# Performance work log

Measured on AMD Instinct MI355X. Metric: run time of the kernel, lower is better.

## Reference

```python
import jax, jax.numpy as jnp
import numpy as np

N_SRC, N_DST, K, T = 16384, 8192, 16, 2
NODE_IN, EDGE_IN, TIME_D = 128, 64, 128
D_MODEL = NODE_IN + TIME_D + EDGE_IN  # 320
N_HEAD, D_K = 8, 64                   # d_k = d_v
HID = 128
LN_EPS = 1e-5


def setup_inputs() -> dict:
    key = jax.random.key(0)
    ks = jax.random.split(key, 10)
    std_qk = np.sqrt(2.0 / (D_MODEL + D_K)).astype(np.float32)
    return {
        "node_features": jax.random.normal(ks[0], (N_SRC, NODE_IN), jnp.float32),
        "edge_features": jax.random.normal(ks[1], (N_DST, K, T, EDGE_IN), jnp.float32),
        "delta_t": jax.random.uniform(ks[2], (N_DST, K, T), jnp.float32) * 100.0,
        "neigh_idx": jax.random.randint(ks[3], (N_DST, K), 0, N_SRC),
        "basis_freq": jnp.asarray(1.0 / 10 ** np.linspace(0, 9, TIME_D), jnp.float32),
        "phase": jnp.zeros((TIME_D,), jnp.float32),
        "w_qs": jax.random.normal(ks[4], (N_HEAD * D_K, D_MODEL), jnp.float32) * std_qk,
        "w_ks": jax.random.normal(ks[5], (N_HEAD * D_K, D_MODEL), jnp.float32) * std_qk,
        "w_vs": jax.random.normal(ks[6], (N_HEAD * D_K, D_MODEL), jnp.float32) * std_qk,
        "fc_w": jax.random.normal(ks[7], (D_MODEL, N_HEAD * D_K), jnp.float32) * 0.03,
        "fc_b": jnp.zeros((D_MODEL,), jnp.float32),
        "ln_g": jnp.ones((D_MODEL,), jnp.float32),
        "ln_b": jnp.zeros((D_MODEL,), jnp.float32),
        "node_w": jax.random.normal(ks[8], (HID, 2 * NODE_IN + TIME_D + EDGE_IN), jnp.float32) * 0.05,
        "node_b": jnp.zeros((HID,), jnp.float32),
    }


def reference(node_features, edge_features, delta_t, neigh_idx, basis_freq, phase,
              w_qs, w_ks, w_vs, fc_w, fc_b, ln_g, ln_b, node_w, node_b):
    h_dst = node_features[:N_DST]                                  # [N, NODE_IN]
    # message_func: per-edge time encoding + gather src feats + concat
    te = jnp.cos(delta_t[..., None] * basis_freq + phase)          # [N, K, T, TIME_D]
    h_nb = node_features[neigh_idx]                                # [N, K, NODE_IN] (irregular gather)
    h_nb = jnp.broadcast_to(h_nb[:, :, None, :], (N_DST, K, T, NODE_IN))
    m = jnp.concatenate([h_nb, edge_features, te], axis=-1)        # [N, K, T, D_MODEL]
    m = m.reshape(N_DST, K * T, D_MODEL)                           # mailbox kv
    # reduce_func query: [h_dst, zeros(edge_in), time_encode(0)=cos(phase)]
    t0 = jnp.broadcast_to(jnp.cos(phase), (N_DST, TIME_D))
    q = jnp.concatenate([h_dst, jnp.zeros((N_DST, EDGE_IN), h_dst.dtype), t0], axis=-1)  # [N, D_MODEL]
    # multi-head attention (len_q = 1)
    qh = (q @ w_qs.T).reshape(N_DST, N_HEAD, D_K)
    kh = (m @ w_ks.T).reshape(N_DST, K * T, N_HEAD, D_K)
    vh = (m @ w_vs.T).reshape(N_DST, K * T, N_HEAD, D_K)
    scores = jnp.einsum('nhd,nlhd->nhl', qh, kh) / np.float32(np.sqrt(D_K))
    attn = jax.nn.softmax(scores, axis=-1)
    ctx = jnp.einsum('nhl,nlhd->nhd', attn, vh).reshape(N_DST, N_HEAD * D_K)
    out = ctx @ fc_w.T + fc_b
    x = out + q                                                    # residual
    mu = x.mean(-1, keepdims=True)
    var = x.var(-1, keepdims=True)
    h_neigh = ln_g * (x - mu) * jax.lax.rsqrt(var + LN_EPS) + ln_b  # layer norm
    h = jnp.concatenate([h_dst, h_neigh], axis=-1)                 # [N, 2*NODE_IN+TIME_D+EDGE_IN]
    return jax.nn.relu(h @ node_w.T + node_b)                      # [N, HID]
```

## Files before the change

### kernel.cpp

```cpp
#include <hip/hip_runtime.h>
#include <math.h>

#define LNB      32
#define NODE_IN  128
#define EDGE_IN  64
#define TIME_D   128
#define D_MODEL  320
#define N_HEAD   8
#define D_K      64
#define NHD      512
#define HID      128
#define IN2      448
#define N_DSTN   8192

typedef __attribute__((ext_vector_type(8))) short bf16x8;
typedef __attribute__((ext_vector_type(4))) float f32x4;
#define MFMA16(a,b,c) __builtin_amdgcn_mfma_f32_16x16x32_bf16(a,b,c,0,0,0)

#define WS_WQ    0
#define WS_WKT   163840
#define WS_WV    327680
#define WS_FCW   491520
#define WS_NW    655360
#define WS_QKM   712704

__device__ __forceinline__ unsigned short f2bf(float f) {
  union { float f; unsigned i; } v; v.f = f;
  unsigned x = v.i;
  return (unsigned short)((x + 0x7fffu + ((x >> 16) & 1u)) >> 16);
}

__global__ __launch_bounds__(256)
void prep_weights(const float* __restrict__ wq, const float* __restrict__ wk,
                  const float* __restrict__ wv, const float* __restrict__ fcw,
                  const float* __restrict__ nw, unsigned short* __restrict__ ws)
{
  int i = blockIdx.x * 256 + threadIdx.x;
  ws[WS_WQ + i] = f2bf(wq[i]);
  {
    int h = i / 20480, r = i - h * 20480, d = r >> 6, dk = r & 63;
    ws[WS_WKT + i] = f2bf(wk[(size_t)(h * 64 + dk) * D_MODEL + d]);
  }
  ws[WS_WV + i] = f2bf(wv[i]);
  ws[WS_FCW + i] = f2bf(fcw[i]);
  if (i < HID * IN2) ws[WS_NW + i] = f2bf(nw[i]);
}

__global__ __launch_bounds__(256, 4)
void tgat_qk(const float* __restrict__ nf, const float* __restrict__ ph,
             const unsigned short* __restrict__ ws, unsigned short* __restrict__ qkm)
{
  __shared__ alignas(16) unsigned short sQ[16 * 328];
  __shared__ alignas(16) unsigned short sQH[16 * 520];
  __shared__ float cph[TIME_D];

  const int tid = threadIdx.x;
  const int wid = tid >> 6, lane = tid & 63, qd = lane >> 4, lm = lane & 15;
  const int n0 = blockIdx.x * 16;
  const unsigned short* wsWQ  = ws + WS_WQ;
  const unsigned short* wsWKT = ws + WS_WKT;

  if (tid < TIME_D) cph[tid] = __cosf(ph[tid]);
  __syncthreads();
  for (int k = 0; k < 20; ++k) {
    int idx = k * 256 + tid;
    int n = idx / D_MODEL, d = idx - n * D_MODEL;
    float v;
    if (d < NODE_IN)      v = nf[(size_t)(n0 + n) * NODE_IN + d];
    else if (d < 192)     v = 0.f;
    else                  v = cph[d - 192];
    sQ[n * 328 + d] = f2bf(v);
  }
  __syncthreads();

  {
    f32x4 acc[8] = {};
    for (int kt = 0; kt < 10; ++kt) {
      bf16x8 a = *(const bf16x8*)&sQ[lm * 328 + kt * 32 + qd * 8];
      #pragma unroll
      for (int u = 0; u < 8; ++u) {
        int j = (wid * 8 + u) * 16 + lm;
        bf16x8 b = *(const bf16x8*)&wsWQ[(size_t)j * D_MODEL + kt * 32 + qd * 8];
        acc[u] = MFMA16(a, b, acc[u]);
      }
    }
    #pragma unroll
    for (int u = 0; u < 8; ++u)
      #pragma unroll
      for (int r = 0; r < 4; ++r)
        sQH[(qd * 4 + r) * 520 + (wid * 8 + u) * 16 + lm] = f2bf(acc[u][r]);
  }
  __syncthreads();

  #pragma unroll
  for (int t = 0; t < 2; ++t) {
    const int h = wid + 4 * t;
    bf16x8 a0 = *(const bf16x8*)&sQH[lm * 520 + h * 64 + qd * 8];
    bf16x8 a1 = *(const bf16x8*)&sQH[lm * 520 + h * 64 + 32 + qd * 8];
    for (int dt = 0; dt < 20; ++dt) {
      int d = dt * 16 + lm;
      bf16x8 b0 = *(const bf16x8*)&wsWKT[((size_t)h * D_MODEL + d) * 64 + qd * 8];
      bf16x8 b1 = *(const bf16x8*)&wsWKT[((size_t)h * D_MODEL + d) * 64 + 32 + qd * 8];
      f32x4 acc = {};
      acc = MFMA16(a0, b0, acc);
      acc = MFMA16(a1, b1, acc);
      #pragma unroll
      for (int r = 0; r < 4; ++r)
        qkm[(size_t)(n0 + qd * 4 + r) * 2560 + h * D_MODEL + d] = f2bf(acc[r]);
    }
  }
}

__global__ __launch_bounds__(256, 3)
void tgat_attn(const float* __restrict__ nf, const float* __restrict__ ef,
               const float* __restrict__ dtp, const int* __restrict__ nidx,
               const float* __restrict__ freq, const float* __restrict__ ph,
               unsigned short* __restrict__ qkm)
{
  __shared__ alignas(16) unsigned short sM [LNB * 328];
  __shared__ alignas(16) unsigned short sMT[D_MODEL * 40];
  __shared__ alignas(16) unsigned short sATT[16 * 40];
  __shared__ float sFP[TIME_D], sPH[TIME_D], sDT[LNB];
  __shared__ int   sNI[16];

  const int tid = threadIdx.x;
  const int wid = tid >> 6, lane = tid & 63, qd = lane >> 4, lm = lane & 15;
  const int n = blockIdx.x;

  if (tid < TIME_D) { sFP[tid] = freq[tid]; sPH[tid] = ph[tid]; }
  if (tid < 16)  sNI[tid] = nidx[n * 16 + tid];
  if (tid < LNB) sDT[tid] = dtp[(size_t)n * LNB + tid];
  __syncthreads();

  #pragma unroll 1
  for (int it = 0; it < 5; ++it) {
    int g = it * 256 + tid;
    int l = g & 31, dg = g >> 5;
    int d0 = dg * 8;
    float v[8];
    if (dg < 16) {
      const float4* src = (const float4*)(nf + (size_t)sNI[l >> 1] * NODE_IN + d0);
      float4 f0 = src[0], f1 = src[1];
      v[0]=f0.x; v[1]=f0.y; v[2]=f0.z; v[3]=f0.w; v[4]=f1.x; v[5]=f1.y; v[6]=f1.z; v[7]=f1.w;
    } else if (dg < 24) {
      const float4* src = (const float4*)(ef + ((size_t)n * LNB + l) * EDGE_IN + (d0 - NODE_IN));
      float4 f0 = src[0], f1 = src[1];
      v[0]=f0.x; v[1]=f0.y; v[2]=f0.z; v[3]=f0.w; v[4]=f1.x; v[5]=f1.y; v[6]=f1.z; v[7]=f1.w;
    } else {
      int dd = d0 - 192;
      float dt = sDT[l];
      #pragma unroll
      for (int j = 0; j < 8; ++j) v[j] = __cosf(dt * sFP[dd + j] + sPH[dd + j]);
    }
    unsigned short b8[8];
    #pragma unroll
    for (int j = 0; j < 8; ++j) b8[j] = f2bf(v[j]);
    *(bf16x8*)&sM[l * 328 + d0] = *(const bf16x8*)b8;
    #pragma unroll
    for (int j = 0; j < 8; ++j) sMT[(d0 + j) * 40 + l] = b8[j];
  }
  __syncthreads();

  if (wid == 0) {
    const unsigned short* qn = qkm + (size_t)n * 2560;
    f32x4 acc0 = {}, acc1 = {};
    for (int kt = 0; kt < 10; ++kt) {
      bf16x8 b = {0,0,0,0,0,0,0,0};
      if (lm < 8) b = *(const bf16x8*)&qn[lm * D_MODEL + kt * 32 + qd * 8];
      bf16x8 a0 = *(const bf16x8*)&sM[lm * 328 + kt * 32 + qd * 8];
      bf16x8 a1 = *(const bf16x8*)&sM[(16 + lm) * 328 + kt * 32 + qd * 8];
      acc0 = MFMA16(a0, b, acc0);
      acc1 = MFMA16(a1, b, acc1);
    }
    float s[8], e[8];
    #pragma unroll
    for (int r = 0; r < 4; ++r) { s[r] = acc0[r] * 0.125f; s[4 + r] = acc1[r] * 0.125f; }
    float mx = s[0];
    #pragma unroll
    for (int i = 1; i < 8; ++i) mx = fmaxf(mx, s[i]);
    mx = fmaxf(mx, __shfl_xor(mx, 16));
    mx = fmaxf(mx, __shfl_xor(mx, 32));
    float sum = 0.f;
    #pragma unroll
    for (int i = 0; i < 8; ++i) { e[i] = __expf(s[i] - mx); sum += e[i]; }
    sum += __shfl_xor(sum, 16);
    sum += __shfl_xor(sum, 32);
    float inv = 1.f / sum;
    #pragma unroll
    for (int i = 0; i < 8; ++i) {
      int l = (i < 4) ? (qd * 4 + i) : (16 + qd * 4 + (i - 4));
      sATT[lm * 40 + l] = f2bf(e[i] * inv);
    }
  }
  __syncthreads();

  {
    bf16x8 a = *(const bf16x8*)&sATT[lm * 40 + qd * 8];
    for (int dt = wid; dt < 20; dt += 4) {
      int d = dt * 16 + lm;
      bf16x8 b = *(const bf16x8*)&sMT[d * 40 + qd * 8];
      f32x4 acc = {};
      acc = MFMA16(a, b, acc);
      if (qd < 2) {
        #pragma unroll
        for (int r = 0; r < 4; ++r)
          qkm[(size_t)n * 2560 + (qd * 4 + r) * D_MODEL + d] = f2bf(acc[r]);
      }
    }
  }
}

__global__ __launch_bounds__(256, 3)
void tgat_post(const float* __restrict__ nf, const float* __restrict__ ph,
               const float* __restrict__ fcb, const float* __restrict__ lng,
               const float* __restrict__ lnb_, const float* __restrict__ nbias,
               const unsigned short* __restrict__ ws,
               const unsigned short* __restrict__ qkm, float* __restrict__ out)
{
  __shared__ alignas(16) unsigned short sCtx[16 * 520];
  __shared__ alignas(16) float sX[16 * 321];
  __shared__ alignas(16) unsigned short sXb[16 * 328];
  __shared__ alignas(16) unsigned short sQb[16 * 136];
  __shared__ float cph[TIME_D];

  const int tid = threadIdx.x;
  const int wid = tid >> 6, lane = tid & 63, qd = lane >> 4, lm = lane & 15;
  const int n0 = blockIdx.x * 16;
  const unsigned short* wsWV  = ws + WS_WV;
  const unsigned short* wsFCW = ws + WS_FCW;
  const unsigned short* wsNW  = ws + WS_NW;

  if (tid < TIME_D) cph[tid] = __cosf(ph[tid]);
  {
    int nn = tid >> 4, k0 = (tid & 15) * 8;
    const float4* src = (const float4*)(nf + (size_t)(n0 + nn) * NODE_IN + k0);
    float4 f0 = src[0], f1 = src[1];
    unsigned short b8[8] = { f2bf(f0.x), f2bf(f0.y), f2bf(f0.z), f2bf(f0.w),
                             f2bf(f1.x), f2bf(f1.y), f2bf(f1.z), f2bf(f1.w) };
    *(bf16x8*)&sQb[nn * 136 + k0] = *(const bf16x8*)b8;
  }

  #pragma unroll
  for (int t = 0; t < 2; ++t) {
    const int h = wid + 4 * t;
    f32x4 acc[4] = {};
    for (int kt = 0; kt < 10; ++kt) {
      bf16x8 a = *(const bf16x8*)&qkm[(size_t)(n0 + lm) * 2560 + h * D_MODEL + kt * 32 + qd * 8];
      #pragma unroll
      for (int u = 0; u < 4; ++u) {
        int jv = h * 64 + u * 16 + lm;
        bf16x8 b = *(const bf16x8*)&wsWV[(size_t)jv * D_MODEL + kt * 32 + qd * 8];
        acc[u] = MFMA16(a, b, acc[u]);
      }
    }
    #pragma unroll
    for (int u = 0; u < 4; ++u)
      #pragma unroll
      for (int r = 0; r < 4; ++r)
        sCtx[(qd * 4 + r) * 520 + h * 64 + u * 16 + lm] = f2bf(acc[u][r]);
  }
  __syncthreads();

  {
    f32x4 acc[5] = {};
    for (int ks = 0; ks < 16; ++ks) {
      bf16x8 a = *(const bf16x8*)&sCtx[lm * 520 + ks * 32 + qd * 8];
      #pragma unroll
      for (int u = 0; u < 5; ++u) {
        int c = (wid + 4 * u) * 16 + lm;
        bf16x8 b = *(const bf16x8*)&wsFCW[(size_t)c * NHD + ks * 32 + qd * 8];
        acc[u] = MFMA16(a, b, acc[u]);
      }
    }
    #pragma unroll
    for (int u = 0; u < 5; ++u) {
      int c = (wid + 4 * u) * 16 + lm;
      float fb = fcb[c];
      #pragma unroll
      for (int r = 0; r < 4; ++r) {
        int nn = qd * 4 + r;
        float qv;
        if (c < NODE_IN)      qv = nf[(size_t)(n0 + nn) * NODE_IN + c];
        else if (c < 192)     qv = 0.f;
        else                  qv = cph[c - 192];
        sX[nn * 321 + c] = acc[u][r] + fb + qv;
      }
    }
  }
  __syncthreads();

  #pragma unroll
  for (int t = 0; t < 4; ++t) {
    int nn = wid * 4 + t;
    float v[5], s = 0.f, s2 = 0.f;
    #pragma unroll
    for (int i = 0; i < 5; ++i) {
      v[i] = sX[nn * 321 + lane + 64 * i];
      s += v[i]; s2 += v[i] * v[i];
    }
    #pragma unroll
    for (int off = 32; off >= 1; off >>= 1) { s += __shfl_xor(s, off); s2 += __shfl_xor(s2, off); }
    float mean = s * (1.f / D_MODEL);
    float var  = s2 * (1.f / D_MODEL) - mean * mean;
    float rstd = rsqrtf(var + 1e-5f);
    #pragma unroll
    for (int i = 0; i < 5; ++i) {
      int c = lane + 64 * i;
      sXb[nn * 328 + c] = f2bf(lng[c] * ((v[i] - mean) * rstd) + lnb_[c]);
    }
  }
  __syncthreads();

  #pragma unroll
  for (int t = 0; t < 2; ++t) {
    int o = (wid + 4 * t) * 16 + lm;
    f32x4 acc = {};
    for (int ks = 0; ks < 14; ++ks) {
      bf16x8 a;
      if (ks < 4) a = *(const bf16x8*)&sQb[lm * 136 + ks * 32 + qd * 8];
      else        a = *(const bf16x8*)&sXb[lm * 328 + (ks - 4) * 32 + qd * 8];
      bf16x8 b = *(const bf16x8*)&wsNW[(size_t)o * IN2 + ks * 32 + qd * 8];
      acc = MFMA16(a, b, acc);
    }
    float nbv = nbias[o];
    #pragma unroll
    for (int r = 0; r < 4; ++r)
      out[(size_t)(n0 + qd * 4 + r) * HID + o] = fmaxf(acc[r] + nbv, 0.f);
  }
}

extern "C" void kernel_launch(void* const* d_in, const int* in_sizes, int n_in,
                              void* d_out, int out_size, void* d_ws, size_t ws_size,
                              hipStream_t stream) {
  const float* nf   = (const float*)d_in[0];
  const float* ef   = (const float*)d_in[1];
  const float* dtp  = (const float*)d_in[2];
  const int*   nidx = (const int*)  d_in[3];
  const float* freq = (const float*)d_in[4];
  const float* ph   = (const float*)d_in[5];
  const float* wq   = (const float*)d_in[6];
  const float* wk   = (const float*)d_in[7];
  const float* wv   = (const float*)d_in[8];
  const float* fcw  = (const float*)d_in[9];
  const float* fcb  = (const float*)d_in[10];
  const float* lng  = (const float*)d_in[11];
  const float* lnb_ = (const float*)d_in[12];
  const float* nw   = (const float*)d_in[13];
  const float* nb   = (const float*)d_in[14];
  float* out = (float*)d_out;
  unsigned short* ws = (unsigned short*)d_ws;
  unsigned short* qkm = ws + WS_QKM;

  prep_weights<<<640, 256, 0, stream>>>(wq, wk, wv, fcw, nw, ws);
  tgat_qk   <<<512,  256, 0, stream>>>(nf, ph, ws, qkm);
  tgat_attn <<<8192, 256, 0, stream>>>(nf, ef, dtp, nidx, freq, ph, qkm);
  tgat_post <<<512,  256, 0, stream>>>(nf, ph, fcb, lng, lnb_, nb, ws, qkm, out);
}
```

Before: 299.6 us.

## Fold weight products algebraically: precompute Wq·Wk, fc·Wv, LN gains into weights

Precomputes combined weight matrices so the query-key projection becomes one GEMM over the 128 nonzero query features plus a constant bias, and value projection and fc merge into one 2560-wide GEMM per node. LayerNorm gain and bias are folded into the node-MLP weights and bias. The attention kernel drops the transposed mailbox copy and computes the context with scalar FMAs from shared memory. The post kernel uses 32-row tiles with 512 threads and a cross-wave LN reduction. The trade-off is a much larger post GEMM (K=2560) and new weight-prep kernels that run on every call, plus bf16 rounding of the fused weight products.

```diff
diff --git a/kernel.cpp b/kernel.cpp
--- a/kernel.cpp
+++ b/kernel.cpp
@@ -17,126 +17,185 @@
 typedef __attribute__((ext_vector_type(4))) float f32x4;
 #define MFMA16(a,b,c) __builtin_amdgcn_mfma_f32_16x16x32_bf16(a,b,c,0,0,0)
 
-#define WS_WQ    0
-#define WS_WKT   163840
-#define WS_WV    327680
-#define WS_FCW   491520
-#define WS_NW    655360
-#define WS_QKM   712704
+#define WS_QKM   0
+#define WS_WQK   20971520
+#define WS_WVF   21299200
+#define WS_NWC   22118400
+#define WS_F32   22175744
+#define F_C0     0
+#define F_C0K    512
+#define F_CC     3072
+#define F_B2     3392
 
 __device__ __forceinline__ unsigned short f2bf(float f) {
   union { float f; unsigned i; } v; v.f = f;
   unsigned x = v.i;
   return (unsigned short)((x + 0x7fffu + ((x >> 16) & 1u)) >> 16);
 }
+__device__ __forceinline__ float2 bf2f2(unsigned u) {
+  union { unsigned i; float f; } lo, hi;
+  lo.i = u << 16; hi.i = u & 0xffff0000u;
+  return make_float2(lo.f, hi.f);
+}
+__device__ __forceinline__ void up8(uint4 v, float* o) {
+  float2 a = bf2f2(v.x), b = bf2f2(v.y), c = bf2f2(v.z), d = bf2f2(v.w);
+  o[0]=a.x; o[1]=a.y; o[2]=b.x; o[3]=b.y; o[4]=c.x; o[5]=c.y; o[6]=d.x; o[7]=d.y;
+}
+__device__ __forceinline__ bf16x8 pack8(const float* v) {
+  unsigned short b8[8];
+  #pragma unroll
+  for (int j = 0; j < 8; ++j) b8[j] = f2bf(v[j]);
+  return *(const bf16x8*)b8;
+}
 
 __global__ __launch_bounds__(256)
-void prep_weights(const float* __restrict__ wq, const float* __restrict__ wk,
-                  const float* __restrict__ wv, const float* __restrict__ fcw,
-                  const float* __restrict__ nw, unsigned short* __restrict__ ws)
+void prep1(const float* __restrict__ wq, const float* __restrict__ lng,
+           const float* __restrict__ lnb_, const float* __restrict__ nw,
+           const float* __restrict__ nb, const float* __restrict__ fcb,
+           const float* __restrict__ ph, unsigned short* __restrict__ ws)
 {
   int i = blockIdx.x * 256 + threadIdx.x;
-  ws[WS_WQ + i] = f2bf(wq[i]);
+  unsigned short* nwc = ws + WS_NWC;
+  float* f32r = (float*)(ws + WS_F32);
+  if (i < 16384) {
+    int o = i >> 7, k = i & 127;
+    nwc[o * IN2 + k] = f2bf(nw[(size_t)o * IN2 + k]);
+  } else if (i < 57344) {
+    int j = i - 16384, o = j / 320, c = j - o * 320;
+    nwc[o * IN2 + 128 + c] = f2bf(nw[(size_t)o * IN2 + 128 + c] * lng[c]);
+  } else if (i < 57856) {
+    int j = i - 57344;
+    float s = 0.f;
+    for (int k = 0; k < 128; ++k) s += __cosf(ph[k]) * wq[(size_t)j * D_MODEL + 192 + k];
+    f32r[F_C0 + j] = s;
+  } else if (i < 58176) {
+    int c = i - 57856;
+    f32r[F_CC + c] = fcb[c] + (c >= 192 ? __cosf(ph[c - 192]) : 0.f);
+  } else if (i < 58304) {
+    int o = i - 58176;
+    float s = nb[o];
+    for (int c = 0; c < 320; ++c) s += nw[(size_t)o * IN2 + 128 + c] * lnb_[c];
+    f32r[F_B2 + o] = s;
+  }
+}
+
+__global__ __launch_bounds__(256)
+void prep2(const float* __restrict__ wq, const float* __restrict__ wk,
+           const float* __restrict__ wv, const float* __restrict__ fcw,
+           unsigned short* __restrict__ ws)
+{
+  int i = blockIdx.x * 256 + threadIdx.x;
+  float* f32r = (float*)(ws + WS_F32);
+  if (i < 327680) {
+    int hd = i >> 7, k = i & 127;
+    int h = hd / 320, d = hd - h * 320;
+    const float* wqb = wq + (size_t)h * 64 * D_MODEL + k;
+    const float* wkb = wk + (size_t)h * 64 * D_MODEL + d;
+    float s = 0.f;
+    for (int dk = 0; dk < 64; ++dk) s += wqb[(size_t)dk * D_MODEL] * wkb[(size_t)dk * D_MODEL];
+    ws[WS_WQK + (size_t)hd * 128 + k] = f2bf(s);
+  } else if (i < 330240) {
+    int hd = i - 327680;
+    int h = hd / 320, d = hd - h * 320;
+    float s = 0.f;
+    for (int dk = 0; dk < 64; ++dk)
+      s += f32r[F_C0 + h * 64 + dk] * wk[(size_t)(h * 64 + dk) * D_MODEL + d];
+    f32r[F_C0K + hd] = s;
+  } else if (i < 1149440) {
+    int j = i - 330240;
+    int c = j / 2560, hd = j - c * 2560;
+    int h = hd / 320, d = hd - h * 320;
+    const float* fb  = fcw + (size_t)c * NHD + h * 64;
+    const float* wvb = wv + (size_t)h * 64 * D_MODEL + d;
+    float s = 0.f;
+    for (int jj = 0; jj < 64; ++jj) s += fb[jj] * wvb[(size_t)jj * D_MODEL];
+    ws[WS_WVF + (size_t)c * 2560 + hd] = f2bf(s);
+  }
+}
+
+__global__ __launch_bounds__(256, 6)
+void tgat_qk(const float* __restrict__ nf, const unsigned short* __restrict__ ws,
+             unsigned short* __restrict__ qkm)
+{
+  __shared__ alignas(16) unsigned short sA[64 * 136];
+  const int tid = threadIdx.x, wid = tid >> 6, lane = tid & 63, qd = lane >> 4, lm = lane & 15;
+  const int mt_blk = blockIdx.x / 20, nt_blk = blockIdx.x - mt_blk * 20;
+  const int n0 = mt_blk * 64, c0 = nt_blk * 128;
+  const unsigned short* wqk = ws + WS_WQK;
+  const float* f32r = (const float*)(ws + WS_F32);
+
   {
-    int h = i / 20480, r = i - h * 20480, d = r >> 6, dk = r & 63;
-    ws[WS_WKT + i] = f2bf(wk[(size_t)(h * 64 + dk) * D_MODEL + d]);
-  }
-  ws[WS_WV + i] = f2bf(wv[i]);
-  ws[WS_FCW + i] = f2bf(fcw[i]);
-  if (i < HID * IN2) ws[WS_NW + i] = f2bf(nw[i]);
-}
-
-__global__ __launch_bounds__(256, 4)
-void tgat_qk(const float* __restrict__ nf, const float* __restrict__ ph,
-             const unsigned short* __restrict__ ws, unsigned short* __restrict__ qkm)
-{
-  __shared__ alignas(16) unsigned short sQ[16 * 328];
-  __shared__ alignas(16) unsigned short sQH[16 * 520];
-  __shared__ float cph[TIME_D];
-
-  const int tid = threadIdx.x;
-  const int wid = tid >> 6, lane = tid & 63, qd = lane >> 4, lm = lane & 15;
-  const int n0 = blockIdx.x * 16;
-  const unsigned short* wsWQ  = ws + WS_WQ;
-  const unsigned short* wsWKT = ws + WS_WKT;
-
-  if (tid < TIME_D) cph[tid] = __cosf(ph[tid]);
-  __syncthreads();
-  for (int k = 0; k < 20; ++k) {
-    int idx = k * 256 + tid;
-    int n = idx / D_MODEL, d = idx - n * D_MODEL;
-    float v;
-    if (d < NODE_IN)      v = nf[(size_t)(n0 + n) * NODE_IN + d];
-    else if (d < 192)     v = 0.f;
-    else                  v = cph[d - 192];
-    sQ[n * 328 + d] = f2bf(v);
-  }
-  __syncthreads();
-
-  {
-    f32x4 acc[8] = {};
-    for (int kt = 0; kt < 10; ++kt) {
-      bf16x8 a = *(const bf16x8*)&sQ[lm * 328 + kt * 32 + qd * 8];
+    int n = tid >> 2, k0 = (tid & 3) * 32;
+    const float4* src = (const float4*)(nf + (size_t)(n0 + n) * NODE_IN + k0);
+    #pragma unroll
+    for (int q = 0; q < 4; ++q) {
+      float4 f0 = src[2 * q], f1 = src[2 * q + 1];
+      float v[8] = {f0.x, f0.y, f0.z, f0.w, f1.x, f1.y, f1.z, f1.w};
+      *(bf16x8*)&sA[n * 136 + k0 + q * 8] = pack8(v);
+    }
+  }
+  __syncthreads();
+
+  f32x4 acc[2][4] = {};
+  for (int kt = 0; kt < 4; ++kt) {
+    bf16x8 a[4];
+    #pragma unroll
+    for (int mt = 0; mt < 4; ++mt)
+      a[mt] = *(const bf16x8*)&sA[(mt * 16 + lm) * 136 + kt * 32 + qd * 8];
+    #pragma unroll
+    for (int t = 0; t < 2; ++t) {
+      int cg = c0 + (2 * wid + t) * 16 + lm;
+      bf16x8 b = *(const bf16x8*)&wqk[(size_t)cg * 128 + kt * 32 + qd * 8];
       #pragma unroll
-      for (int u = 0; u < 8; ++u) {
-        int j = (wid * 8 + u) * 16 + lm;
-        bf16x8 b = *(const bf16x8*)&wsWQ[(size_t)j * D_MODEL + kt * 32 + qd * 8];
-        acc[u] = MFMA16(a, b, acc[u]);
-      }
-    }
-    #pragma unroll
-    for (int u = 0; u < 8; ++u)
+      for (int mt = 0; mt < 4; ++mt) acc[t][mt] = MFMA16(a[mt], b, acc[t][mt]);
+    }
+  }
+  #pragma unroll
+  for (int t = 0; t < 2; ++t) {
+    int cg = c0 + (2 * wid + t) * 16 + lm;
+    float ck = f32r[F_C0K + cg];
+    #pragma unroll
+    for (int mt = 0; mt < 4; ++mt)
       #pragma unroll
       for (int r = 0; r < 4; ++r)
-        sQH[(qd * 4 + r) * 520 + (wid * 8 + u) * 16 + lm] = f2bf(acc[u][r]);
-  }
-  __syncthreads();
-
-  #pragma unroll
-  for (int t = 0; t < 2; ++t) {
-    const int h = wid + 4 * t;
-    bf16x8 a0 = *(const bf16x8*)&sQH[lm * 520 + h * 64 + qd * 8];
-    bf16x8 a1 = *(const bf16x8*)&sQH[lm * 520 + h * 64 + 32 + qd * 8];
-    for (int dt = 0; dt < 20; ++dt) {
-      int d = dt * 16 + lm;
-      bf16x8 b0 = *(const bf16x8*)&wsWKT[((size_t)h * D_MODEL + d) * 64 + qd * 8];
-      bf16x8 b1 = *(const bf16x8*)&wsWKT[((size_t)h * D_MODEL + d) * 64 + 32 + qd * 8];
-      f32x4 acc = {};
-      acc = MFMA16(a0, b0, acc);
-      acc = MFMA16(a1, b1, acc);
-      #pragma unroll
-      for (int r = 0; r < 4; ++r)
-        qkm[(size_t)(n0 + qd * 4 + r) * 2560 + h * D_MODEL + d] = f2bf(acc[r]);
-    }
-  }
-}
-
-__global__ __launch_bounds__(256, 3)
+        qkm[(size_t)(n0 + mt * 16 + qd * 4 + r) * 2560 + cg] = f2bf(acc[t][mt][r] + ck);
+  }
+}
+
+__global__ __launch_bounds__(256, 5)
 void tgat_attn(const float* __restrict__ nf, const float* __restrict__ ef,
                const float* __restrict__ dtp, const int* __restrict__ nidx,
                const float* __restrict__ freq, const float* __restrict__ ph,
                unsigned short* __restrict__ qkm)
 {
-  __shared__ alignas(16) unsigned short sM [LNB * 328];
-  __shared__ alignas(16) unsigned short sMT[D_MODEL * 40];
-  __shared__ alignas(16) unsigned short sATT[16 * 40];
+  __shared__ alignas(16) unsigned short sM[LNB * 328];
+  __shared__ float sATTf[8 * 36];
   __shared__ float sFP[TIME_D], sPH[TIME_D], sDT[LNB];
-  __shared__ int   sNI[16];
-
-  const int tid = threadIdx.x;
-  const int wid = tid >> 6, lane = tid & 63, qd = lane >> 4, lm = lane & 15;
+  __shared__ int sNI[16];
+
+  const int tid = threadIdx.x, wid = tid >> 6, lane = tid & 63, qd = lane >> 4, lm = lane & 15;
   const int n = blockIdx.x;
+  unsigned short* qn = qkm + (size_t)n * 2560;
 
   if (tid < TIME_D) { sFP[tid] = freq[tid]; sPH[tid] = ph[tid]; }
-  if (tid < 16)  sNI[tid] = nidx[n * 16 + tid];
+  if (tid < 16) sNI[tid] = nidx[n * 16 + tid];
   if (tid < LNB) sDT[tid] = dtp[(size_t)n * LNB + tid];
-  __syncthreads();
-
-  #pragma unroll 1
+
+  bf16x8 qkB[10];
+  if (wid == 0) {
+    #pragma unroll
+    for (int kt = 0; kt < 10; ++kt) {
+      bf16x8 z = {0,0,0,0,0,0,0,0};
+      qkB[kt] = z;
+      if (lm < 8) qkB[kt] = *(const bf16x8*)&qn[lm * 320 + kt * 32 + qd * 8];
+    }
+  }
+  __syncthreads();
+
+  #pragma unroll
   for (int it = 0; it < 5; ++it) {
     int g = it * 256 + tid;
-    int l = g & 31, dg = g >> 5;
-    int d0 = dg * 8;
+    int l = g & 31, dg = g >> 5, d0 = dg * 8;
     float v[8];
     if (dg < 16) {
       const float4* src = (const float4*)(nf + (size_t)sNI[l >> 1] * NODE_IN + d0);
@@ -152,25 +211,17 @@
       #pragma unroll
       for (int j = 0; j < 8; ++j) v[j] = __cosf(dt * sFP[dd + j] + sPH[dd + j]);
     }
-    unsigned short b8[8];
-    #pragma unroll
-    for (int j = 0; j < 8; ++j) b8[j] = f2bf(v[j]);
-    *(bf16x8*)&sM[l * 328 + d0] = *(const bf16x8*)b8;
-    #pragma unroll
-    for (int j = 0; j < 8; ++j) sMT[(d0 + j) * 40 + l] = b8[j];
+    *(bf16x8*)&sM[l * 328 + d0] = pack8(v);
   }
   __syncthreads();
 
   if (wid == 0) {
-    const unsigned short* qn = qkm + (size_t)n * 2560;
     f32x4 acc0 = {}, acc1 = {};
     for (int kt = 0; kt < 10; ++kt) {
-      bf16x8 b = {0,0,0,0,0,0,0,0};
-      if (lm < 8) b = *(const bf16x8*)&qn[lm * D_MODEL + kt * 32 + qd * 8];
       bf16x8 a0 = *(const bf16x8*)&sM[lm * 328 + kt * 32 + qd * 8];
       bf16x8 a1 = *(const bf16x8*)&sM[(16 + lm) * 328 + kt * 32 + qd * 8];
-      acc0 = MFMA16(a0, b, acc0);
-      acc1 = MFMA16(a1, b, acc1);
+      acc0 = MFMA16(a0, qkB[kt], acc0);
+      acc1 = MFMA16(a1, qkB[kt], acc1);
     }
     float s[8], e[8];
     #pragma unroll
@@ -189,143 +240,134 @@
     #pragma unroll
     for (int i = 0; i < 8; ++i) {
       int l = (i < 4) ? (qd * 4 + i) : (16 + qd * 4 + (i - 4));
-      sATT[lm * 40 + l] = f2bf(e[i] * inv);
-    }
-  }
-  __syncthreads();
-
-  {
-    bf16x8 a = *(const bf16x8*)&sATT[lm * 40 + qd * 8];
-    for (int dt = wid; dt < 20; dt += 4) {
-      int d = dt * 16 + lm;
-      bf16x8 b = *(const bf16x8*)&sMT[d * 40 + qd * 8];
-      f32x4 acc = {};
-      acc = MFMA16(a, b, acc);
-      if (qd < 2) {
-        #pragma unroll
-        for (int r = 0; r < 4; ++r)
-          qkm[(size_t)n * 2560 + (qd * 4 + r) * D_MODEL + d] = f2bf(acc[r]);
-      }
-    }
-  }
-}
-
-__global__ __launch_bounds__(256, 3)
-void tgat_post(const float* __restrict__ nf, const float* __restrict__ ph,
-               const float* __restrict__ fcb, const float* __restrict__ lng,
-               const float* __restrict__ lnb_, const float* __restrict__ nbias,
-               const unsigned short* __restrict__ ws,
+      if (lm < 8) sATTf[lm * 36 + l] = e[i] * inv;
+    }
+  }
+  __syncthreads();
+
+  for (int item = tid; item < 320; item += 256) {
+    int h = item / 40, c = item - h * 40;
+    const float* att = &sATTf[h * 36];
+    float a[8] = {};
+    int rot = tid & 31;
+    for (int ll = 0; ll < LNB; ++ll) {
+      int l = (ll + rot) & 31;
+      float at = att[l];
+      float mv[8]; up8(*(const uint4*)&sM[l * 328 + c * 8], mv);
+      #pragma unroll
+      for (int j = 0; j < 8; ++j) a[j] += at * mv[j];
+    }
+    *(bf16x8*)&qn[h * 320 + c * 8] = pack8(a);
+  }
+}
+
+__global__ __launch_bounds__(512, 2)
+void tgat_post(const float* __restrict__ nf, const unsigned short* __restrict__ ws,
                const unsigned short* __restrict__ qkm, float* __restrict__ out)
 {
-  __shared__ alignas(16) unsigned short sCtx[16 * 520];
-  __shared__ alignas(16) float sX[16 * 321];
-  __shared__ alignas(16) unsigned short sXb[16 * 328];
-  __shared__ alignas(16) unsigned short sQb[16 * 136];
-  __shared__ float cph[TIME_D];
-
-  const int tid = threadIdx.x;
-  const int wid = tid >> 6, lane = tid & 63, qd = lane >> 4, lm = lane & 15;
-  const int n0 = blockIdx.x * 16;
-  const unsigned short* wsWV  = ws + WS_WV;
-  const unsigned short* wsFCW = ws + WS_FCW;
-  const unsigned short* wsNW  = ws + WS_NW;
-
-  if (tid < TIME_D) cph[tid] = __cosf(ph[tid]);
+  __shared__ alignas(16) unsigned short sQb[32 * 136];
+  __shared__ alignas(16) unsigned short sXb[32 * 328];
+  __shared__ float sRed[8][4][4][2];
+  __shared__ float sStat[32][2];
+
+  const int tid = threadIdx.x, wid = tid >> 6, lane = tid & 63, qd = lane >> 4, lm = lane & 15;
+  const int n0 = blockIdx.x * 32;
+  const int mt = wid & 1, ws4 = wid >> 1;
+  const unsigned short* wvf = ws + WS_WVF;
+  const unsigned short* nwc = ws + WS_NWC;
+  const float* f32r = (const float*)(ws + WS_F32);
+
   {
     int nn = tid >> 4, k0 = (tid & 15) * 8;
     const float4* src = (const float4*)(nf + (size_t)(n0 + nn) * NODE_IN + k0);
     float4 f0 = src[0], f1 = src[1];
-    unsigned short b8[8] = { f2bf(f0.x), f2bf(f0.y), f2bf(f0.z), f2bf(f0.w),
-                             f2bf(f1.x), f2bf(f1.y), f2bf(f1.z), f2bf(f1.w) };
-    *(bf16x8*)&sQb[nn * 136 + k0] = *(const bf16x8*)b8;
-  }
-
-  #pragma unroll
-  for (int t = 0; t < 2; ++t) {
-    const int h = wid + 4 * t;
-    f32x4 acc[4] = {};
-    for (int kt = 0; kt < 10; ++kt) {
-      bf16x8 a = *(const bf16x8*)&qkm[(size_t)(n0 + lm) * 2560 + h * D_MODEL + kt * 32 + qd * 8];
-      #pragma unroll
-      for (int u = 0; u < 4; ++u) {
-        int jv = h * 64 + u * 16 + lm;
-        bf16x8 b = *(const bf16x8*)&wsWV[(size_t)jv * D_MODEL + kt * 32 + qd * 8];
-        acc[u] = MFMA16(a, b, acc[u]);
-      }
-    }
-    #pragma unroll
-    for (int u = 0; u < 4; ++u)
+    float v[8] = {f0.x, f0.y, f0.z, f0.w, f1.x, f1.y, f1.z, f1.w};
+    *(bf16x8*)&sQb[nn * 136 + k0] = pack8(v);
+  }
+
+  f32x4 acc[5] = {};
+  const unsigned short* arow = qkm + (size_t)(n0 + mt * 16 + lm) * 2560;
+  for (int kt = 0; kt < 80; ++kt) {
+    bf16x8 a = *(const bf16x8*)&arow[kt * 32 + qd * 8];
+    #pragma unroll
+    for (int u = 0; u < 5; ++u) {
+      int c = (ws4 + 4 * u) * 16 + lm;
+      bf16x8 b = *(const bf16x8*)&wvf[(size_t)c * 2560 + kt * 32 + qd * 8];
+      acc[u] = MFMA16(a, b, acc[u]);
+    }
+  }
+
+  float val[5][4];
+  float s1[4] = {}, s2[4] = {};
+  #pragma unroll
+  for (int u = 0; u < 5; ++u) {
+    int t = ws4 + 4 * u, c = t * 16 + lm;
+    float ccv = f32r[F_CC + c];
+    #pragma unroll
+    for (int r = 0; r < 4; ++r) {
+      float v = acc[u][r] + ccv;
+      if (t < 8) v += nf[(size_t)(n0 + mt * 16 + qd * 4 + r) * NODE_IN + c];
+      val[u][r] = v;
+      s1[r] += v; s2[r] += v * v;
+    }
+  }
+  #pragma unroll
+  for (int off = 1; off <= 8; off <<= 1) {
+    #pragma unroll
+    for (int r = 0; r < 4; ++r) {
+      s1[r] += __shfl_xor(s1[r], off);
+      s2[r] += __shfl_xor(s2[r], off);
+    }
+  }
+  if (lm == 0) {
+    #pragma unroll
+    for (int r = 0; r < 4; ++r) { sRed[wid][qd][r][0] = s1[r]; sRed[wid][qd][r][1] = s2[r]; }
+  }
+  __syncthreads();
+  if (tid < 32) {
+    int m2 = tid >> 4, rr = tid & 15, q = rr >> 2, r = rr & 3;
+    float S = 0.f, S2 = 0.f;
+    #pragma unroll
+    for (int j = 0; j < 4; ++j) { S += sRed[2 * j + m2][q][r][0]; S2 += sRed[2 * j + m2][q][r][1]; }
+    float mean = S * (1.f / D_MODEL);
+    float var = S2 * (1.f / D_MODEL) - mean * mean;
+    sStat[tid][0] = mean;
+    sStat[tid][1] = rsqrtf(var + 1e-5f);
+  }
+  __syncthreads();
+  #pragma unroll
+  for (int u = 0; u < 5; ++u) {
+    int c = (ws4 + 4 * u) * 16 + lm;
+    #pragma unroll
+    for (int r = 0; r < 4; ++r) {
+      int row = mt * 16 + qd * 4 + r;
+      float xh = (val[u][r] - sStat[row][0]) * sStat[row][1];
+      sXb[row * 328 + c] = f2bf(xh);
+    }
+  }
+  __syncthreads();
+
+  f32x4 oacc[2] = {};
+  for (int kt = 0; kt < 14; ++kt) {
+    bf16x8 a[2];
+    #pragma unroll
+    for (int m2 = 0; m2 < 2; ++m2) {
+      if (kt < 4) a[m2] = *(const bf16x8*)&sQb[(m2 * 16 + lm) * 136 + kt * 32 + qd * 8];
+      else        a[m2] = *(const bf16x8*)&sXb[(m2 * 16 + lm) * 328 + (kt - 4) * 32 + qd * 8];
+    }
+    int o = wid * 16 + lm;
+    bf16x8 b = *(const bf16x8*)&nwc[(size_t)o * IN2 + kt * 32 + qd * 8];
+    oacc[0] = MFMA16(a[0], b, oacc[0]);
+    oacc[1] = MFMA16(a[1], b, oacc[1]);
+  }
+  {
+    int o = wid * 16 + lm;
+    float bz = f32r[F_B2 + o];
+    #pragma unroll
+    for (int m2 = 0; m2 < 2; ++m2)
       #pragma unroll
       for (int r = 0; r < 4; ++r)
-        sCtx[(qd * 4 + r) * 520 + h * 64 + u * 16 + lm] = f2bf(acc[u][r]);
-  }
-  __syncthreads();
-
-  {
-    f32x4 acc[5] = {};
-    for (int ks = 0; ks < 16; ++ks) {
-      bf16x8 a = *(const bf16x8*)&sCtx[lm * 520 + ks * 32 + qd * 8];
-      #pragma unroll
-      for (int u = 0; u < 5; ++u) {
-        int c = (wid + 4 * u) * 16 + lm;
-        bf16x8 b = *(const bf16x8*)&wsFCW[(size_t)c * NHD + ks * 32 + qd * 8];
-        acc[u] = MFMA16(a, b, acc[u]);
-      }
-    }
-    #pragma unroll
-    for (int u = 0; u < 5; ++u) {
-      int c = (wid + 4 * u) * 16 + lm;
-      float fb = fcb[c];
-      #pragma unroll
-      for (int r = 0; r < 4; ++r) {
-        int nn = qd * 4 + r;
-        float qv;
-        if (c < NODE_IN)      qv = nf[(size_t)(n0 + nn) * NODE_IN + c];
-        else if (c < 192)     qv = 0.f;
-        else                  qv = cph[c - 192];
-        sX[nn * 321 + c] = acc[u][r] + fb + qv;
-      }
-    }
-  }
-  __syncthreads();
-
-  #pragma unroll
-  for (int t = 0; t < 4; ++t) {
-    int nn = wid * 4 + t;
-    float v[5], s = 0.f, s2 = 0.f;
-    #pragma unroll
-    for (int i = 0; i < 5; ++i) {
-      v[i] = sX[nn * 321 + lane + 64 * i];
-      s += v[i]; s2 += v[i] * v[i];
-    }
-    #pragma unroll
-    for (int off = 32; off >= 1; off >>= 1) { s += __shfl_xor(s, off); s2 += __shfl_xor(s2, off); }
-    float mean = s * (1.f / D_MODEL);
-    float var  = s2 * (1.f / D_MODEL) - mean * mean;
-    float rstd = rsqrtf(var + 1e-5f);
-    #pragma unroll
-    for (int i = 0; i < 5; ++i) {
-      int c = lane + 64 * i;
-      sXb[nn * 328 + c] = f2bf(lng[c] * ((v[i] - mean) * rstd) + lnb_[c]);
-    }
-  }
-  __syncthreads();
-
-  #pragma unroll
-  for (int t = 0; t < 2; ++t) {
-    int o = (wid + 4 * t) * 16 + lm;
-    f32x4 acc = {};
-    for (int ks = 0; ks < 14; ++ks) {
-      bf16x8 a;
-      if (ks < 4) a = *(const bf16x8*)&sQb[lm * 136 + ks * 32 + qd * 8];
-      else        a = *(const bf16x8*)&sXb[lm * 328 + (ks - 4) * 32 + qd * 8];
-      bf16x8 b = *(const bf16x8*)&wsNW[(size_t)o * IN2 + ks * 32 + qd * 8];
-      acc = MFMA16(a, b, acc);
-    }
-    float nbv = nbias[o];
-    #pragma unroll
-    for (int r = 0; r < 4; ++r)
-      out[(size_t)(n0 + qd * 4 + r) * HID + o] = fmaxf(acc[r] + nbv, 0.f);
+        out[(size_t)(n0 + m2 * 16 + qd * 4 + r) * HID + o] = fmaxf(oacc[m2][r] + bz, 0.f);
   }
 }
 
@@ -351,8 +393,9 @@
   unsigned short* ws = (unsigned short*)d_ws;
   unsigned short* qkm = ws + WS_QKM;
 
-  prep_weights<<<640, 256, 0, stream>>>(wq, wk, wv, fcw, nw, ws);
-  tgat_qk   <<<512,  256, 0, stream>>>(nf, ph, ws, qkm);
-  tgat_attn <<<8192, 256, 0, stream>>>(nf, ef, dtp, nidx, freq, ph, qkm);
-  tgat_post <<<512,  256, 0, stream>>>(nf, ph, fcb, lng, lnb_, nb, ws, qkm, out);
-}
+  prep1<<<228, 256, 0, stream>>>(wq, lng, lnb_, nw, nb, fcb, ph, ws);
+  prep2<<<4490, 256, 0, stream>>>(wq, wk, wv, fcw, ws);
+  tgat_qk  <<<2560, 256, 0, stream>>>(nf, ws, qkm);
+  tgat_attn<<<8192, 256, 0, stream>>>(nf, ef, dtp, nidx, freq, ph, qkm);
+  tgat_post<<<256,  512, 0, stream>>>(nf, ws, qkm, out);
+}
```

After: 630.2 us. 110% more time.
